# Performance work log

Hardware: AMD Instinct MI355X
Metric: run time of the kernel (lower is better)

The kernel has to match this reference:

```python
import jax, jax.numpy as jnp
import numpy as np

B = 64           # graphs
NPG = 2048       # nodes per graph
N = B * NPG      # total nodes
EPG = 32768      # edges per graph (avg degree 16)
E = B * EPG
D = 32           # in_features == out_features
RATIO = 0.5
K = int(NPG * RATIO)  # nodes kept per graph


def setup_inputs() -> dict:
    key = jax.random.key(0)
    ks = jax.random.split(key, 12)
    x = jax.random.normal(ks[0], (N, D), dtype=jnp.float32)
    gid = jnp.repeat(jnp.arange(B, dtype=jnp.int32), EPG)
    src = gid * NPG + jax.random.randint(ks[1], (E,), 0, NPG, dtype=jnp.int32)
    dst = gid * NPG + jax.random.randint(ks[2], (E,), 0, NPG, dtype=jnp.int32)
    edge_index = jnp.stack([src, dst])                      # [2, E]
    edge_attr = jax.random.uniform(ks[3], (E,), dtype=jnp.float32)
    batch = jnp.repeat(jnp.arange(B, dtype=jnp.int32), NPG)  # [N]
    s = 1.0 / np.sqrt(D)
    params = {}
    for i in range(3):
        params[f"W_root{i+1}"] = jax.random.normal(ks[4 + 2 * i], (D, D), dtype=jnp.float32) * s
        params[f"W_rel{i+1}"] = jax.random.normal(ks[5 + 2 * i], (D, D), dtype=jnp.float32) * s
        params[f"b{i+1}"] = jnp.zeros((D,), dtype=jnp.float32)
    return {"x": x, "edge_index": edge_index, "edge_attr": edge_attr, "batch": batch, **params}


def _graph_conv(x, src, dst, W_root, W_rel, b):
    # PyG GraphConv (aggr='add'): out_i = W_root x_i + W_rel * sum_{j->i} x_j + b
    agg = jax.ops.segment_sum(x[src], dst, num_segments=N)  # [N, D]
    return x @ W_root + agg @ W_rel + b


def reference(x, edge_index, edge_attr, batch,
              W_root1, W_rel1, b1, W_root2, W_rel2, b2, W_root3, W_rel3, b3):
    src, dst = edge_index[0], edge_index[1]
    x2 = _graph_conv(x, src, dst, W_root1, W_rel1, b1)  # [N, D]
    y2 = _graph_conv(x, src, dst, W_root2, W_rel2, b2)  # [N, D]
    # per-node attention score = <x2_i, y2_i> / sqrt(D)
    score = jnp.sum(x2 * y2, axis=-1) / jnp.sqrt(jnp.float32(D))  # [N]
    # topk per graph (equal-size graphs -> reshape + lax.top_k)
    _, top_idx = jax.lax.top_k(score.reshape(B, NPG), K)          # [B, K]
    perm = (top_idx + (jnp.arange(B, dtype=top_idx.dtype) * NPG)[:, None]).reshape(-1)  # [B*K]
    x3 = _graph_conv(x, src, dst, W_root3, W_rel3, b3)            # dropout_rate=0 -> identity
    # skip connection
    x5 = x[perm] + score[perm][:, None] * x3[perm]                # [B*K, D]
    new_batch = batch[perm]
    # filter_adj: relabel surviving nodes, mask (pad with -1 / 0) edges with a dropped endpoint
    new_idx = jnp.full((N,), -1, dtype=jnp.int32).at[perm].set(jnp.arange(perm.shape[0], dtype=jnp.int32))
    ns, nd = new_idx[src], new_idx[dst]
    valid = (ns >= 0) & (nd >= 0)
    new_edge_index = jnp.where(valid[None, :], jnp.stack([ns, nd]), -1)  # [2, E], -1 = dropped
    new_edge_attr = jnp.where(valid, edge_attr, 0.0)
    return (x5, new_edge_index, new_edge_attr, new_batch, perm, score[perm])
```

## Files before the change

### kernel.cpp

```cpp
#include <hip/hip_runtime.h>
#include <hip/hip_bf16.h>

#define NB   64
#define NPG  2048
#define NN   (NB*NPG)
#define EPG  32768
#define EE   (NB*EPG)
#define DD   32
#define KK   1024

typedef unsigned long long u64;
typedef unsigned int u32;

__global__ __launch_bounds__(1024) void build_kernel(
    const int* __restrict__ src, const int* __restrict__ dst,
    int* __restrict__ counts, int* __restrict__ offsets,
    int* __restrict__ edge_ids)
{
    __shared__ int cnt[NPG];
    __shared__ int tot[1024];
    int b = blockIdx.x;
    int t = threadIdx.x;

    for (int i = t; i < NPG; i += 1024) cnt[i] = 0;
    __syncthreads();

    const int ebase = b * EPG;
    const int nbase = b * NPG;

    int dl[32], sl[32];
#pragma unroll
    for (int q = 0; q < 32; q++) {
        int e = ebase + q * 1024 + t;
        dl[q] = dst[e] - nbase;
        sl[q] = src[e];
        atomicAdd(&cnt[dl[q]], 1);
    }
    __syncthreads();

    int c0 = cnt[2*t], c1 = cnt[2*t+1];
    tot[t] = c0 + c1;
    __syncthreads();
    for (int o = 1; o < 1024; o <<= 1) {
        int v = tot[t];
        int u = (t >= o) ? tot[t - o] : 0;
        __syncthreads();
        tot[t] = v + u;
        __syncthreads();
    }
    int excl = (t == 0) ? 0 : tot[t - 1];

    counts[nbase + 2*t]     = c0;
    counts[nbase + 2*t + 1] = c1;
    offsets[nbase + 2*t]     = ebase + excl;
    offsets[nbase + 2*t + 1] = ebase + excl + c0;
    cnt[2*t]     = excl;
    cnt[2*t + 1] = excl + c0;
    __syncthreads();

#pragma unroll
    for (int q = 0; q < 32; q++) {
        int pos = atomicAdd(&cnt[dl[q]], 1);
        edge_ids[ebase + pos] = sl[q];
    }
}

__global__ __launch_bounds__(256) void agg_kernel(
    const float* __restrict__ x,
    const int* __restrict__ counts, const int* __restrict__ offsets,
    const int* __restrict__ edge_ids,
    float* __restrict__ agg)
{
    int b = blockIdx.x;
    int c = (b & 7) * 512 + (b >> 3);
    int tid = c * 256 + threadIdx.x;
    int node = tid >> 3;
    int ch = (tid & 7) * 4;
    int deg  = counts[node];
    int base = offsets[node];
    float ax = 0.f, ay = 0.f, az = 0.f, aw = 0.f;
    for (int k = 0; k < deg; k++) {
        int s = edge_ids[base + k];
        float4 v = *(const float4*)(x + (long long)s * DD + ch);
        ax += v.x; ay += v.y; az += v.z; aw += v.w;
    }
    float4 r; r.x = ax; r.y = ay; r.z = az; r.w = aw;
    *(float4*)(agg + (long long)node * DD + ch) = r;
}

__global__ __launch_bounds__(256) void score_kernel(
    const float* __restrict__ x, const float* __restrict__ agg,
    const float* __restrict__ Wr1, const float* __restrict__ Wl1, const float* __restrict__ b1,
    const float* __restrict__ Wr2, const float* __restrict__ Wl2, const float* __restrict__ b2,
    float* __restrict__ score)
{
    __shared__ float4 sWr1[DD*DD/4], sWl1[DD*DD/4], sWr2[DD*DD/4], sWl2[DD*DD/4];
    __shared__ float sb1[DD], sb2[DD];
    __shared__ float2 part[128];
    {
        int t = threadIdx.x;
        sWr1[t] = ((const float4*)Wr1)[t];
        sWl1[t] = ((const float4*)Wl1)[t];
        sWr2[t] = ((const float4*)Wr2)[t];
        sWl2[t] = ((const float4*)Wl2)[t];
        if (t < DD) { sb1[t] = b1[t]; sb2[t] = b2[t]; }
    }
    __syncthreads();

    int lane = threadIdx.x & 127;
    int half = threadIdx.x >> 7;
    int i0 = blockIdx.x * 128 + lane;
    int i1 = i0 + NN/2;

    float xv0[DD], av0[DD], xv1[DD], av1[DD];
    {
        const float4* xp0 = (const float4*)(x + (long long)i0 * DD);
        const float4* ap0 = (const float4*)(agg + (long long)i0 * DD);
        const float4* xp1 = (const float4*)(x + (long long)i1 * DD);
        const float4* ap1 = (const float4*)(agg + (long long)i1 * DD);
#pragma unroll
        for (int q = 0; q < 8; q++) {
            float4 v0 = xp0[q]; xv0[4*q]=v0.x; xv0[4*q+1]=v0.y; xv0[4*q+2]=v0.z; xv0[4*q+3]=v0.w;
            float4 w0 = ap0[q]; av0[4*q]=w0.x; av0[4*q+1]=w0.y; av0[4*q+2]=w0.z; av0[4*q+3]=w0.w;
            float4 v1 = xp1[q]; xv1[4*q]=v1.x; xv1[4*q+1]=v1.y; xv1[4*q+2]=v1.z; xv1[4*q+3]=v1.w;
            float4 w1 = ap1[q]; av1[4*q]=w1.x; av1[4*q+1]=w1.y; av1[4*q+2]=w1.z; av1[4*q+3]=w1.w;
        }
    }

    float sc0 = 0.f, sc1 = 0.f;
    int dbase = half * 4;
    for (int dd = 0; dd < 4; dd++) {
        int d0 = dbase + dd;
        float a0[4], q0[4], a1[4], q1[4];
#pragma unroll
        for (int j = 0; j < 4; j++) {
            a0[j] = sb1[4*d0+j]; q0[j] = sb2[4*d0+j];
            a1[j] = sb1[4*d0+j]; q1[j] = sb2[4*d0+j];
        }
#pragma unroll
        for (int k = 0; k < DD; k++) {
            float4 wr1 = sWr1[k*8 + d0];
            float4 wl1 = sWl1[k*8 + d0];
            float4 wr2 = sWr2[k*8 + d0];
            float4 wl2 = sWl2[k*8 + d0];
            const float* r1 = &wr1.x; const float* l1 = &wl1.x;
            const float* r2 = &wr2.x; const float* l2 = &wl2.x;
            float xk0 = xv0[k], ak0 = av0[k];
            float xk1 = xv1[k], ak1 = av1[k];
#pragma unroll
            for (int j = 0; j < 4; j++) {
                a0[j] += xk0 * r1[j];
                a0[j] += ak0 * l1[j];
                q0[j] += xk0 * r2[j];
                q0[j] += ak0 * l2[j];
                a1[j] += xk1 * r1[j];
                a1[j] += ak1 * l1[j];
                q1[j] += xk1 * r2[j];
                q1[j] += ak1 * l2[j];
            }
        }
#pragma unroll
        for (int j = 0; j < 4; j++) { sc0 += a0[j] * q0[j]; sc1 += a1[j] * q1[j]; }
    }

    if (half) { part[lane].x = sc0; part[lane].y = sc1; }
    __syncthreads();
    if (!half) {
        float2 p = part[lane];
        score[i0] = (sc0 + p.x) * 0.17677669529663687f;
        score[i1] = (sc1 + p.y) * 0.17677669529663687f;
    }
}

__global__ __launch_bounds__(1024) void topk_kernel(
    const float* __restrict__ score,
    int* __restrict__ perm_int, int* __restrict__ new_idx,
    float* __restrict__ out_perm,
    float* __restrict__ out_batch,
    float* __restrict__ out_score)
{
    __shared__ u64 keys[NPG];
    int b = blockIdx.x;
    int t = threadIdx.x;
    const float* s = score + (long long)b * NPG;

    for (int j = t; j < NPG; j += 1024) {
        u32 u = __float_as_uint(s[j]);
        u32 h = (u & 0x80000000u) ? u : ~(u | 0x80000000u);
        keys[j] = ((u64)h << 32) | (u32)j;
    }

    for (int k = 2; k <= NPG; k <<= 1) {
        for (int j = k >> 1; j > 0; j >>= 1) {
            __syncthreads();
            int i = ((t & ~(j - 1)) << 1) | (t & (j - 1));
            int l = i | j;
            u64 a = keys[i], c = keys[l];
            bool up = ((i & k) == 0);
            if ((a > c) == up) { keys[i] = c; keys[l] = a; }
        }
    }
    __syncthreads();

    u64 kk = keys[t];
    int idx = (int)(u32)(kk & 0xFFFFFFFFu);
    int g = b * NPG + idx;
    int o = b * KK + t;
    perm_int[o] = g;
    new_idx[g] = o;
    out_perm[o]  = (float)g;
    out_batch[o] = (float)b;
    out_score[o] = s[idx];

    u64 kd = keys[t + KK];
    int idxd = (int)(u32)(kd & 0xFFFFFFFFu);
    new_idx[b * NPG + idxd] = -1;
}

__global__ __launch_bounds__(256) void x5_kernel(
    const float* __restrict__ x, const float* __restrict__ agg,
    const float* __restrict__ Wr3, const float* __restrict__ Wl3, const float* __restrict__ b3,
    const int* __restrict__ perm_int, const float* __restrict__ score,
    float* __restrict__ out_x5)
{
    __shared__ float4 sWr[DD*DD/4], sWl[DD*DD/4];
    __shared__ float sb[DD];
    {
        int t = threadIdx.x;
        sWr[t] = ((const float4*)Wr3)[t];
        sWl[t] = ((const float4*)Wl3)[t];
        if (t < DD) sb[t] = b3[t];
    }
    __syncthreads();

    int lane = threadIdx.x & 127;
    int half = threadIdx.x >> 7;
    int i = blockIdx.x * 128 + lane;
    int g = perm_int[i];
    float sc = score[g];

    float xv[DD], av[DD];
    {
        const float4* xp = (const float4*)(x + (long long)g * DD);
        const float4* ap = (const float4*)(agg + (long long)g * DD);
#pragma unroll
        for (int q = 0; q < 8; q++) {
            float4 v = xp[q]; xv[4*q]=v.x; xv[4*q+1]=v.y; xv[4*q+2]=v.z; xv[4*q+3]=v.w;
            float4 w = ap[q]; av[4*q]=w.x; av[4*q+1]=w.y; av[4*q+2]=w.z; av[4*q+3]=w.w;
        }
    }

    float* outp = out_x5 + (long long)i * DD;
    int dbase = half * 4;
    for (int dd = 0; dd < 4; dd++) {
        int d0 = dbase + dd;
        float a[4];
#pragma unroll
        for (int j = 0; j < 4; j++) a[j] = sb[4*d0+j];
#pragma unroll
        for (int k = 0; k < DD; k++) {
            float xk = xv[k], ak = av[k];
            float4 wr = sWr[k*8 + d0];
            float4 wl = sWl[k*8 + d0];
            const float* rp = &wr.x; const float* lp = &wl.x;
#pragma unroll
            for (int j = 0; j < 4; j++) {
                a[j] += xk * rp[j];
                a[j] += ak * lp[j];
            }
        }
#pragma unroll
        for (int j = 0; j < 4; j++) outp[4*d0+j] = xv[4*d0+j] + sc * a[j];
    }
}

__global__ __launch_bounds__(256) void edge_kernel(
    const int* __restrict__ src, const int* __restrict__ dst,
    const float* __restrict__ edge_attr,
    const int* __restrict__ new_idx,
    float* __restrict__ out_ei,
    float* __restrict__ out_attr)
{
    int e = (blockIdx.x * 256 + threadIdx.x) * 4;
    if (e >= EE) return;
    int4 s4 = *(const int4*)(src + e);
    int4 d4 = *(const int4*)(dst + e);
    float4 at = *(const float4*)(edge_attr + e);

    int ns[4] = { new_idx[s4.x], new_idx[s4.y], new_idx[s4.z], new_idx[s4.w] };
    int nd[4] = { new_idx[d4.x], new_idx[d4.y], new_idx[d4.z], new_idx[d4.w] };
    float av[4] = { at.x, at.y, at.z, at.w };

    float4 os, od, oa;
    float* osp = &os.x; float* odp = &od.x; float* oap = &oa.x;
#pragma unroll
    for (int j = 0; j < 4; j++) {
        bool valid = (ns[j] >= 0) && (nd[j] >= 0);
        osp[j] = (float)(valid ? ns[j] : -1);
        odp[j] = (float)(valid ? nd[j] : -1);
        oap[j] = valid ? av[j] : 0.f;
    }
    *(float4*)(out_ei + e)      = os;
    *(float4*)(out_ei + EE + e) = od;
    *(float4*)(out_attr + e)    = oa;
}

extern "C" void kernel_launch(void* const* d_in, const int* in_sizes, int n_in,
                              void* d_out, int out_size, void* d_ws, size_t ws_size,
                              hipStream_t stream)
{
    const float* x     = (const float*)d_in[0];
    const int*   src   = (const int*)d_in[1];
    const int*   dst   = ((const int*)d_in[1]) + EE;
    const float* eattr = (const float*)d_in[2];
    const float* Wr1 = (const float*)d_in[4];
    const float* Wl1 = (const float*)d_in[5];
    const float* b1  = (const float*)d_in[6];
    const float* Wr2 = (const float*)d_in[7];
    const float* Wl2 = (const float*)d_in[8];
    const float* b2  = (const float*)d_in[9];
    const float* Wr3 = (const float*)d_in[10];
    const float* Wl3 = (const float*)d_in[11];
    const float* b3  = (const float*)d_in[12];

    char* ws = (char*)d_ws;
    int*   counts   = (int*)  (ws + 0);
    int*   offsets  = (int*)  (ws + (size_t)NN*4);
    float* score    = (float*)(ws + (size_t)NN*8);
    int*   perm_int = (int*)  (ws + (size_t)NN*12);
    int*   new_idx  = (int*)  (ws + (size_t)NN*12 + (size_t)NB*KK*4);

    float* out = (float*)d_out;
    float* out_x5    = out;
    float* out_ei    = out + (size_t)NB*KK*DD;
    float* out_attr  = out_ei + (size_t)2*EE;
    float* out_batch = out_attr + (size_t)EE;
    float* out_perm  = out_batch + (size_t)NB*KK;
    float* out_score = out_perm + (size_t)NB*KK;

    float* agg      = out_ei;
    int*   edge_ids = (int*)out_attr;

    build_kernel<<<NB, 1024, 0, stream>>>(src, dst, counts, offsets, edge_ids);

    agg_kernel  <<<(NN*8)/256, 256, 0, stream>>>(x, counts, offsets, edge_ids, agg);

    score_kernel<<<NN/256, 256, 0, stream>>>(x, agg, Wr1, Wl1, b1, Wr2, Wl2, b2, score);

    topk_kernel<<<NB, 1024, 0, stream>>>(score, perm_int, new_idx,
                                         out_perm, out_batch, out_score);

    x5_kernel<<<(NB*KK)/128, 256, 0, stream>>>(x, agg, Wr3, Wl3, b3,
                                               perm_int, score, out_x5);

    edge_kernel<<<(EE/4)/256, 256, 0, stream>>>(src, dst, eattr, new_idx, out_ei, out_attr);
}
```

Baseline: 237.4 us.

## Split CSR build into histogram, scan and scatter kernels over 256 blocks

The single per-graph CSR build kernel (64 blocks) is replaced by three kernels. A histogram pass splits each graph's edges into 4 slices across 256 blocks. A scan pass builds counts, offsets and per-slice cursors. A scatter pass uses the cursors to place source ids. The aim is to occupy more CUs than the 64-block launch could. The cost is two extra launches and extra global traffic for the hist and cursor arrays in the workspace.

```diff
diff --git a/kernel.cpp b/kernel.cpp
--- a/kernel.cpp
+++ b/kernel.cpp
@@ -12,33 +12,44 @@
 typedef unsigned long long u64;
 typedef unsigned int u32;
 
-__global__ __launch_bounds__(1024) void build_kernel(
-    const int* __restrict__ src, const int* __restrict__ dst,
-    int* __restrict__ counts, int* __restrict__ offsets,
-    int* __restrict__ edge_ids)
+__global__ __launch_bounds__(1024) void hist_kernel(
+    const int* __restrict__ dst, int* __restrict__ hist)
 {
     __shared__ int cnt[NPG];
-    __shared__ int tot[1024];
     int b = blockIdx.x;
     int t = threadIdx.x;
-
+    int g = b & 63, s = b >> 6;
     for (int i = t; i < NPG; i += 1024) cnt[i] = 0;
     __syncthreads();
-
-    const int ebase = b * EPG;
-    const int nbase = b * NPG;
-
-    int dl[32], sl[32];
-#pragma unroll
-    for (int q = 0; q < 32; q++) {
+    const int ebase = g * EPG + s * 8192;
+    const int nbase = g * NPG;
+#pragma unroll
+    for (int q = 0; q < 8; q++) {
         int e = ebase + q * 1024 + t;
-        dl[q] = dst[e] - nbase;
-        sl[q] = src[e];
-        atomicAdd(&cnt[dl[q]], 1);
-    }
-    __syncthreads();
-
-    int c0 = cnt[2*t], c1 = cnt[2*t+1];
+        atomicAdd(&cnt[dst[e] - nbase], 1);
+    }
+    __syncthreads();
+    int* hb = hist + (s * 64 + g) * NPG;
+    for (int i = t; i < NPG; i += 1024) hb[i] = cnt[i];
+}
+
+__global__ __launch_bounds__(1024) void scan2_kernel(
+    const int* __restrict__ hist,
+    int* __restrict__ counts, int* __restrict__ offsets,
+    int* __restrict__ cursors)
+{
+    __shared__ int tot[1024];
+    int g = blockIdx.x;
+    int t = threadIdx.x;
+    int n0 = 2 * t, n1 = 2 * t + 1;
+    int h0[4], h1[4];
+#pragma unroll
+    for (int s = 0; s < 4; s++) {
+        h0[s] = hist[(s * 64 + g) * NPG + n0];
+        h1[s] = hist[(s * 64 + g) * NPG + n1];
+    }
+    int c0 = h0[0] + h0[1] + h0[2] + h0[3];
+    int c1 = h1[0] + h1[1] + h1[2] + h1[3];
     tot[t] = c0 + c1;
     __syncthreads();
     for (int o = 1; o < 1024; o <<= 1) {
@@ -49,19 +60,39 @@
         __syncthreads();
     }
     int excl = (t == 0) ? 0 : tot[t - 1];
-
-    counts[nbase + 2*t]     = c0;
-    counts[nbase + 2*t + 1] = c1;
-    offsets[nbase + 2*t]     = ebase + excl;
-    offsets[nbase + 2*t + 1] = ebase + excl + c0;
-    cnt[2*t]     = excl;
-    cnt[2*t + 1] = excl + c0;
-    __syncthreads();
-
-#pragma unroll
-    for (int q = 0; q < 32; q++) {
-        int pos = atomicAdd(&cnt[dl[q]], 1);
-        edge_ids[ebase + pos] = sl[q];
+    int nbase = g * NPG;
+    counts[nbase + n0] = c0;
+    counts[nbase + n1] = c1;
+    int off0 = g * EPG + excl;
+    int off1 = off0 + c0;
+    offsets[nbase + n0] = off0;
+    offsets[nbase + n1] = off1;
+    int a0 = off0, a1 = off1;
+#pragma unroll
+    for (int s = 0; s < 4; s++) {
+        cursors[(s * 64 + g) * NPG + n0] = a0; a0 += h0[s];
+        cursors[(s * 64 + g) * NPG + n1] = a1; a1 += h1[s];
+    }
+}
+
+__global__ __launch_bounds__(1024) void scatter_kernel(
+    const int* __restrict__ src, const int* __restrict__ dst,
+    const int* __restrict__ cursors, int* __restrict__ edge_ids)
+{
+    __shared__ int cur[NPG];
+    int b = blockIdx.x;
+    int t = threadIdx.x;
+    int g = b & 63, s = b >> 6;
+    const int* cb = cursors + (s * 64 + g) * NPG;
+    for (int i = t; i < NPG; i += 1024) cur[i] = cb[i];
+    __syncthreads();
+    const int ebase = g * EPG + s * 8192;
+    const int nbase = g * NPG;
+#pragma unroll
+    for (int q = 0; q < 8; q++) {
+        int e = ebase + q * 1024 + t;
+        int pos = atomicAdd(&cur[dst[e] - nbase], 1);
+        edge_ids[pos] = src[e];
     }
 }
 
@@ -329,6 +360,8 @@
     float* score    = (float*)(ws + (size_t)NN*8);
     int*   perm_int = (int*)  (ws + (size_t)NN*12);
     int*   new_idx  = (int*)  (ws + (size_t)NN*12 + (size_t)NB*KK*4);
+    int*   hist     = (int*)  (ws + (size_t)NN*16 + (size_t)NB*KK*4);
+    int*   cursors  = (int*)  (ws + (size_t)NN*32 + (size_t)NB*KK*4);
 
     float* out = (float*)d_out;
     float* out_x5    = out;
@@ -341,7 +374,9 @@
     float* agg      = out_ei;
     int*   edge_ids = (int*)out_attr;
 
-    build_kernel<<<NB, 1024, 0, stream>>>(src, dst, counts, offsets, edge_ids);
+    hist_kernel   <<<256, 1024, 0, stream>>>(dst, hist);
+    scan2_kernel  <<<NB, 1024, 0, stream>>>(hist, counts, offsets, cursors);
+    scatter_kernel<<<256, 1024, 0, stream>>>(src, dst, cursors, edge_ids);
 
     agg_kernel  <<<(NN*8)/256, 256, 0, stream>>>(x, counts, offsets, edge_ids, agg);
 
```

Measured after the change: 223.3 us. 1.06x faster.
